# Optimization experiments

Hardware: AMD Instinct MI355X
Metric: run time of the kernel (lower is better)

Reference implementation:

```python
import jax, jax.numpy as jnp
import numpy as np

N = 12288      # nodes
E = 393216     # edges (avg degree 32)
D_IN = 512
D_H = 256      # interm_dim
D_Z = 64       # latent_dim


def setup_inputs() -> dict:
    key = jax.random.key(0)
    ks = jax.random.split(key, 9)
    X = jax.random.normal(ks[0], (N, D_IN), jnp.float32)
    edge_index = jax.random.randint(ks[1], (2, E), 0, N, dtype=jnp.int64)
    # GCNConv weights (glorot-ish scaling)
    W1 = jax.random.normal(ks[2], (D_IN, D_H), jnp.float32) / np.sqrt(D_IN)
    b1 = jnp.zeros((D_H,), jnp.float32)
    Wmu = jax.random.normal(ks[3], (D_H, D_Z), jnp.float32) / np.sqrt(D_H)
    bmu = jnp.zeros((D_Z,), jnp.float32)
    Wsig = jax.random.normal(ks[4], (D_H, 1), jnp.float32) / np.sqrt(D_H)
    bsig = jnp.zeros((1,), jnp.float32)
    # reparameterization noise (torch: Normal(0,1).sample(mus.size()))
    eps = jax.random.normal(ks[5], (N, D_Z), jnp.float32)
    return {"X": X, "edge_index": edge_index, "W1": W1, "b1": b1,
            "Wmu": Wmu, "bmu": bmu, "Wsig": Wsig, "bsig": bsig, "eps": eps}


def _gcn_conv(h_in, W, b, src, dst, norm):
    # GCNConv: linear transform then symmetric-normalized aggregation with self-loops
    h = h_in @ W + b                                   # [N, F_out]
    msg = h[src] * norm[src, None]                     # gather + scale
    agg = jax.ops.segment_sum(msg, dst, num_segments=N)
    # self-loop contribution: norm_i * norm_i * h_i
    return norm[:, None] * (agg + norm[:, None] * h)


def reference(X, edge_index, W1, b1, Wmu, bmu, Wsig, bsig, eps):
    src, dst = edge_index[0], edge_index[1]
    # degree of A + I (edge weight 1, plus self loop)
    deg = jax.ops.segment_sum(jnp.ones((E,), X.dtype), dst, num_segments=N) + 1.0
    norm = jax.lax.rsqrt(deg)                          # D^{-1/2}

    # encoder
    H = jax.nn.relu(_gcn_conv(X, W1, b1, src, dst, norm))   # [N, D_H]; dropout p=0.0
    mus = _gcn_conv(H, Wmu, bmu, src, dst, norm)            # [N, D_Z]
    logsigma2s = _gcn_conv(H, Wsig, bsig, src, dst, norm)   # [N, 1]

    # reparameterize
    sigmas = jnp.exp(0.5 * logsigma2s)                      # [N, 1]
    Z = mus + sigmas * eps                                  # [N, D_Z]

    # dense decoder
    ZZt = Z @ Z.T                                           # [N, N]
    return ZZt, mus, logsigma2s
```

## Files before the change

### kernel.cpp

```cpp
#include <hip/hip_runtime.h>

#define N_NODES 12288
#define N_EDGES 393216
#define DIN 512
#define DH 256
#define DZ 64

typedef __bf16 bf16x8 __attribute__((ext_vector_type(8)));
typedef float f32x4 __attribute__((ext_vector_type(4)));
typedef unsigned short u16x8 __attribute__((ext_vector_type(8)));

static __device__ __forceinline__ unsigned short f2bf(float f) {
    unsigned int u = __float_as_uint(f);
    unsigned int r = (u + 0x7fffu + ((u >> 16) & 1u)) >> 16;
    return (unsigned short)r;
}
static __device__ __forceinline__ float bf2f(unsigned short u) {
    return __uint_as_float((unsigned int)u << 16);
}

__global__ __launch_bounds__(256) void k_prep(const float* __restrict__ X, unsigned short* __restrict__ Xb,
                                              const float* __restrict__ W1, unsigned short* __restrict__ W1T,
                                              const float* __restrict__ Wmu, unsigned short* __restrict__ WmuT,
                                              const int* __restrict__ dst, int* __restrict__ deg) {
    int b = blockIdx.x;
    if (b < 6144) {
        int i = b * 256 + threadIdx.x;
        float4 v = ((const float4*)X)[i];
        ushort4 o;
        o.x = f2bf(v.x); o.y = f2bf(v.y); o.z = f2bf(v.z); o.w = f2bf(v.w);
        ((ushort4*)Xb)[i] = o;
    } else if (b < 6656) {
        int i = (b - 6144) * 256 + threadIdx.x;
        int c = i >> 9, k = i & 511;
        W1T[i] = f2bf(W1[k * DH + c]);
    } else if (b < 6720) {
        int i = (b - 6656) * 256 + threadIdx.x;
        int c = i >> 8, k = i & 255;
        WmuT[i] = f2bf(Wmu[k * DZ + c]);
    } else {
        int e = (b - 6720) * 256 + threadIdx.x;
        atomicAdd(&deg[dst[e]], 1);
    }
}

__global__ __launch_bounds__(1024) void k_scan(const int* __restrict__ cnt, int* __restrict__ rp,
                                               float* __restrict__ norm, int* __restrict__ cursor) {
    __shared__ int sp[1024];
    int t = threadIdx.x;
    int base = t * 12;
    int loc[12];
    int s = 0;
#pragma unroll
    for (int j = 0; j < 12; ++j) {
        int c = cnt[base + j];
        norm[base + j] = rsqrtf((float)c + 1.0f);
        cursor[base + j] = 0;
        loc[j] = s; s += c;
    }
    sp[t] = s;
    __syncthreads();
    for (int off = 1; off < 1024; off <<= 1) {
        int v = (t >= off) ? sp[t - off] : 0;
        __syncthreads();
        sp[t] += v;
        __syncthreads();
    }
    int pre = (t == 0) ? 0 : sp[t - 1];
#pragma unroll
    for (int j = 0; j < 12; ++j) rp[base + j] = pre + loc[j];
    if (t == 1023) rp[N_NODES] = sp[1023];
}

__global__ __launch_bounds__(512) void k_sg(const unsigned short* __restrict__ Xb,
                                            const unsigned short* __restrict__ W1T,
                                            const float* __restrict__ b1, const float* __restrict__ norm,
                                            unsigned short* __restrict__ g1,
                                            const int* __restrict__ src, const int* __restrict__ dst,
                                            const int* __restrict__ rp, int* __restrict__ cursor,
                                            int* __restrict__ ssrc) {
    if (blockIdx.x < 96) {
        int j = blockIdx.x;
        int wid = threadIdx.x >> 6;
        int lane = threadIdx.x & 63;
        int ln = lane & 15, kg = lane >> 4;
        int rb = (j >> 1) * 256 + (wid >> 1) * 64;
        int cb = (j & 1) * 128 + (wid & 1) * 64;
        f32x4 acc[4][4] = {};
        const unsigned short* xa = Xb + (size_t)(rb + ln) * DIN + kg * 8;
        const unsigned short* wb = W1T + (size_t)(cb + ln) * DIN + kg * 8;
        for (int ks = 0; ks < 16; ++ks) {
            int k0 = ks * 32;
            bf16x8 a[4], b[4];
#pragma unroll
            for (int m = 0; m < 4; ++m) a[m] = *(const bf16x8*)(xa + (size_t)m * 16 * DIN + k0);
#pragma unroll
            for (int n = 0; n < 4; ++n) b[n] = *(const bf16x8*)(wb + (size_t)n * 16 * DIN + k0);
#pragma unroll
            for (int m = 0; m < 4; ++m)
#pragma unroll
                for (int n = 0; n < 4; ++n)
                    acc[m][n] = __builtin_amdgcn_mfma_f32_16x16x32_bf16(a[m], b[n], acc[m][n], 0, 0, 0);
        }
#pragma unroll
        for (int m = 0; m < 4; ++m)
#pragma unroll
            for (int r = 0; r < 4; ++r) {
                int row = rb + m * 16 + kg * 4 + r;
                float ni = norm[row];
#pragma unroll
                for (int n = 0; n < 4; ++n) {
                    int col = cb + n * 16 + ln;
                    g1[(size_t)row * DH + col] = f2bf(ni * (acc[m][n][r] + b1[col]));
                }
            }
    } else {
        int base = (blockIdx.x - 96) * 512 + threadIdx.x;
#pragma unroll
        for (int e = base; e < N_EDGES; e += 192 * 512) {
            int d = dst[e];
            int pos = atomicAdd(&cursor[d], 1);
            ssrc[rp[d] + pos] = src[e];
        }
    }
}

__global__ __launch_bounds__(256) void k_agg1(const unsigned short* __restrict__ g1,
                                              const int* __restrict__ rp, const int* __restrict__ ssrc,
                                              const float* __restrict__ norm, const float* __restrict__ Wsig,
                                              unsigned short* __restrict__ G2, float* __restrict__ tvec,
                                              float* __restrict__ qv) {
    int w = threadIdx.x >> 6;
    int lane = threadIdx.x & 63;
    int half = lane >> 5, lh = lane & 31;
    int i = blockIdx.x * 4 + w;
    int beg = rp[i], end = rp[i + 1];
    int cnt = end - beg;
    int itn = (cnt + 1) >> 1;
    size_t cho = (size_t)lh * 8;
    float a8[8] = {};
    float ssum = 0.f;
#pragma unroll 2
    for (int it = 0; it < itn; ++it) {
        int e = beg + it * 2 + half;
        if (e < end) {
            int s = ssrc[e];
            u16x8 v = *(const u16x8*)(g1 + ((size_t)s << 8) + cho);
            ssum += norm[s];
#pragma unroll
            for (int j = 0; j < 8; ++j) a8[j] += bf2f(v[j]);
        }
    }
    if (half == 0) {
        u16x8 v = *(const u16x8*)(g1 + ((size_t)i << 8) + cho);
#pragma unroll
        for (int j = 0; j < 8; ++j) a8[j] += bf2f(v[j]);
    }
#pragma unroll
    for (int j = 0; j < 8; ++j) a8[j] += __shfl_xor(a8[j], 32);
    ssum += __shfl_xor(ssum, 32);
    float ni = norm[i];
    const float4 ws0 = *(const float4*)(Wsig + cho);
    const float4 ws1 = *(const float4*)(Wsig + cho + 4);
    float g[8];
#pragma unroll
    for (int j = 0; j < 8; ++j) g[j] = ni * fmaxf(ni * a8[j], 0.f);
    float qp = g[0] * ws0.x + g[1] * ws0.y + g[2] * ws0.z + g[3] * ws0.w
             + g[4] * ws1.x + g[5] * ws1.y + g[6] * ws1.z + g[7] * ws1.w;
    if (half == 0) {
        u16x8 o;
#pragma unroll
        for (int j = 0; j < 8; ++j) o[j] = f2bf(g[j]);
        *(u16x8*)(G2 + ((size_t)i << 8) + cho) = o;
    }
#pragma unroll
    for (int m = 16; m >= 1; m >>= 1) qp += __shfl_xor(qp, m);
    if (lane == 0) {
        tvec[i] = ssum + ni;
        qv[i] = qp;
    }
}

__global__ __launch_bounds__(256) void k_gemm2(const unsigned short* __restrict__ G2,
                                               const unsigned short* __restrict__ WmuT,
                                               unsigned short* __restrict__ Pb) {
    int wid = threadIdx.x >> 6;
    int lane = threadIdx.x & 63;
    int ln = lane & 15, kg = lane >> 4;
    int rb = blockIdx.x * 128 + wid * 32;
    f32x4 acc[2][4] = {};
    const unsigned short* xa = G2 + (size_t)(rb + ln) * DH + kg * 8;
    const unsigned short* wb = WmuT + (size_t)ln * DH + kg * 8;
    for (int ks = 0; ks < 8; ++ks) {
        int k0 = ks * 32;
        bf16x8 a[2], b[4];
#pragma unroll
        for (int m = 0; m < 2; ++m) a[m] = *(const bf16x8*)(xa + (size_t)m * 16 * DH + k0);
#pragma unroll
        for (int n = 0; n < 4; ++n) b[n] = *(const bf16x8*)(wb + (size_t)n * 16 * DH + k0);
#pragma unroll
        for (int m = 0; m < 2; ++m)
#pragma unroll
            for (int n = 0; n < 4; ++n)
                acc[m][n] = __builtin_amdgcn_mfma_f32_16x16x32_bf16(a[m], b[n], acc[m][n], 0, 0, 0);
    }
#pragma unroll
    for (int m = 0; m < 2; ++m)
#pragma unroll
        for (int n = 0; n < 4; ++n)
#pragma unroll
            for (int r = 0; r < 4; ++r) {
                int row = rb + m * 16 + kg * 4 + r;
                int col = n * 16 + ln;
                Pb[(size_t)row * DZ + col] = f2bf(acc[m][n][r]);
            }
}

__global__ __launch_bounds__(256) void k_agg2(const unsigned short* __restrict__ Pb,
                                              const float* __restrict__ qv,
                                              const int* __restrict__ rp, const int* __restrict__ ssrc,
                                              const float* __restrict__ norm, const float* __restrict__ tvec,
                                              const float* __restrict__ bmu, const float* __restrict__ bsig,
                                              const float* __restrict__ eps,
                                              float* __restrict__ mus_out, float* __restrict__ logs_out,
                                              unsigned short* __restrict__ Zb) {
    int w = threadIdx.x >> 6;
    int lane = threadIdx.x & 63;
    int grp = lane >> 4, li = lane & 15;
    int i = blockIdx.x * 4 + w;
    int beg = rp[i], end = rp[i + 1];
    int cnt = end - beg;
    int itn = (cnt + 3) >> 2;
    int co = li * 4;
    float a4[4] = {};
    float qa = 0.f;
#pragma unroll 2
    for (int it = 0; it < itn; ++it) {
        int e = beg + it * 4 + grp;
        if (e < end) {
            int s = ssrc[e];
            ushort4 v = *(const ushort4*)(Pb + ((size_t)s << 6) + co);
            qa += qv[s];
            a4[0] += bf2f(v.x); a4[1] += bf2f(v.y); a4[2] += bf2f(v.z); a4[3] += bf2f(v.w);
        }
    }
    if (grp == 0) {
        ushort4 v = *(const ushort4*)(Pb + ((size_t)i << 6) + co);
        qa += qv[i];
        a4[0] += bf2f(v.x); a4[1] += bf2f(v.y); a4[2] += bf2f(v.z); a4[3] += bf2f(v.w);
    }
#pragma unroll
    for (int j = 0; j < 4; ++j) {
        a4[j] += __shfl_xor(a4[j], 16);
        a4[j] += __shfl_xor(a4[j], 32);
    }
    qa += __shfl_xor(qa, 16);
    qa += __shfl_xor(qa, 32);
    float ni = norm[i], tv = tvec[i];
    float ls = ni * (qa + bsig[0] * tv);
    float sig = expf(0.5f * ls);
    if (lane == 0) logs_out[i] = ls;
    if (lane < 16) {
        const float4 bm = *(const float4*)(bmu + co);
        float4 mu;
        mu.x = ni * (a4[0] + bm.x * tv);
        mu.y = ni * (a4[1] + bm.y * tv);
        mu.z = ni * (a4[2] + bm.z * tv);
        mu.w = ni * (a4[3] + bm.w * tv);
        size_t oidx = ((size_t)i << 6) + co;
        *(float4*)(mus_out + oidx) = mu;
        const float4 ep = *(const float4*)(eps + oidx);
        ushort4 z;
        z.x = f2bf(mu.x + sig * ep.x);
        z.y = f2bf(mu.y + sig * ep.y);
        z.z = f2bf(mu.z + sig * ep.z);
        z.w = f2bf(mu.w + sig * ep.w);
        *(ushort4*)(Zb + oidx) = z;
    }
}

#define LPAD 260
__global__ __launch_bounds__(256) void k_zzt(const unsigned short* __restrict__ Zb, float* __restrict__ out) {
    __shared__ float lds[32 * LPAD];
    int w = threadIdx.x >> 6;
    int lane = threadIdx.x & 63;
    int ln = lane & 15, kg = lane >> 4;
    int rb = blockIdx.x * 64;
    int cb = blockIdx.y * 256 + w * 64;
    bf16x8 a[4][2], b[4][2];
#pragma unroll
    for (int m = 0; m < 4; ++m)
#pragma unroll
        for (int kc = 0; kc < 2; ++kc)
            a[m][kc] = *(const bf16x8*)(Zb + (size_t)(rb + m * 16 + ln) * DZ + kc * 32 + kg * 8);
#pragma unroll
    for (int n = 0; n < 4; ++n)
#pragma unroll
        for (int kc = 0; kc < 2; ++kc)
            b[n][kc] = *(const bf16x8*)(Zb + (size_t)(cb + n * 16 + ln) * DZ + kc * 32 + kg * 8);
    f32x4 acc[4][4] = {};
#pragma unroll
    for (int m = 0; m < 4; ++m)
#pragma unroll
        for (int n = 0; n < 4; ++n) {
            acc[m][n] = __builtin_amdgcn_mfma_f32_16x16x32_bf16(a[m][0], b[n][0], acc[m][n], 0, 0, 0);
            acc[m][n] = __builtin_amdgcn_mfma_f32_16x16x32_bf16(a[m][1], b[n][1], acc[m][n], 0, 0, 0);
        }
    int c4 = (threadIdx.x & 63) * 4;
    int rw = threadIdx.x >> 6;
    size_t colbase = (size_t)blockIdx.y * 256 + c4;
#pragma unroll
    for (int p = 0; p < 2; ++p) {
        if (p) __syncthreads();
#pragma unroll
        for (int mm = 0; mm < 2; ++mm) {
            int m = p * 2 + mm;
#pragma unroll
            for (int n = 0; n < 4; ++n)
#pragma unroll
                for (int r = 0; r < 4; ++r)
                    lds[(mm * 16 + kg * 4 + r) * LPAD + w * 64 + n * 16 + ln] = acc[m][n][r];
        }
        __syncthreads();
#pragma unroll
        for (int it = 0; it < 8; ++it) {
            int rl = it * 4 + rw;
            f32x4 v = *(const f32x4*)&lds[rl * LPAD + c4];
            __builtin_nontemporal_store(v, (f32x4*)(out + (size_t)(rb + p * 32 + rl) * N_NODES + colbase));
        }
    }
}

extern "C" void kernel_launch(void* const* d_in, const int* in_sizes, int n_in,
                              void* d_out, int out_size, void* d_ws, size_t ws_size,
                              hipStream_t stream) {
    const float* X = (const float*)d_in[0];
    const int* edge = (const int*)d_in[1];
    const float* W1 = (const float*)d_in[2];
    const float* b1 = (const float*)d_in[3];
    const float* Wmu = (const float*)d_in[4];
    const float* bmu = (const float*)d_in[5];
    const float* Wsig = (const float*)d_in[6];
    const float* bsig = (const float*)d_in[7];
    const float* eps = (const float*)d_in[8];

    const int* esrc = edge;
    const int* edst = edge + N_EDGES;

    char* w = (char*)d_ws;
    int* deg = (int*)w;            w += (size_t)N_NODES * 4;
    int* cursor = (int*)w;         w += (size_t)N_NODES * 4;
    float* norm = (float*)w;       w += (size_t)N_NODES * 4;
    float* tvec = (float*)w;       w += (size_t)N_NODES * 4;
    float* qv = (float*)w;         w += (size_t)N_NODES * 4;
    int* rowptr = (int*)w;         w += (size_t)(N_NODES + 64) * 4;
    int* ssrc = (int*)w;           w += (size_t)N_EDGES * 4;
    unsigned short* Xb = (unsigned short*)w;   w += (size_t)N_NODES * DIN * 2;
    unsigned short* W1T = (unsigned short*)w;  w += (size_t)DIN * DH * 2;
    unsigned short* WmuT = (unsigned short*)w; w += (size_t)DH * DZ * 2;
    unsigned short* g1 = (unsigned short*)w;   w += (size_t)N_NODES * DH * 2;
    unsigned short* G2 = (unsigned short*)w;   w += (size_t)N_NODES * DH * 2;
    unsigned short* Pb = (unsigned short*)w;   w += (size_t)N_NODES * DZ * 2;
    unsigned short* Zb = (unsigned short*)w;   w += (size_t)N_NODES * DZ * 2;

    float* out_zzt = (float*)d_out;
    float* out_mus = out_zzt + (size_t)N_NODES * N_NODES;
    float* out_logs = out_mus + (size_t)N_NODES * DZ;

    (void)hipMemsetAsync(deg, 0, (size_t)N_NODES * 4, stream);
    k_prep<<<8256, 256, 0, stream>>>(X, Xb, W1, W1T, Wmu, WmuT, edst, deg);
    k_scan<<<1, 1024, 0, stream>>>(deg, rowptr, norm, cursor);
    k_sg<<<288, 512, 0, stream>>>(Xb, W1T, b1, norm, g1, esrc, edst, rowptr, cursor, ssrc);
    k_agg1<<<N_NODES / 4, 256, 0, stream>>>(g1, rowptr, ssrc, norm, Wsig, G2, tvec, qv);
    k_gemm2<<<N_NODES / 128, 256, 0, stream>>>(G2, WmuT, Pb);
    k_agg2<<<N_NODES / 4, 256, 0, stream>>>(Pb, qv, rowptr, ssrc, norm, tvec, bmu, bsig, eps,
                                            out_mus, out_logs, Zb);
    k_zzt<<<dim3(N_NODES / 64, N_NODES / 256), 256, 0, stream>>>(Zb, out_zzt);
}
```

Baseline: 267.8 us.

## Fuse layer-1 aggregation with the Wmu projection GEMM via shared memory

The aggregated hidden rows of each block (4 nodes) are staged in LDS instead of being written to a global G2 buffer, and each wave then does a 16x16 MFMA tile of the 256->64 projection directly, writing Pb. This drops one kernel launch and the write and re-read of the N x 256 bf16 intermediate. In exchange, each block does an MFMA on a 16-row tile where only 4 rows are valid, so most of the MFMA work is wasted. WmuT is also re-read from cache by every block, and a block-wide barrier is added after aggregation.

```diff
diff --git a/kernel.cpp b/kernel.cpp
--- a/kernel.cpp
+++ b/kernel.cpp
@@ -125,18 +125,20 @@
     }
 }
 
-__global__ __launch_bounds__(256) void k_agg1(const unsigned short* __restrict__ g1,
-                                              const int* __restrict__ rp, const int* __restrict__ ssrc,
-                                              const float* __restrict__ norm, const float* __restrict__ Wsig,
-                                              unsigned short* __restrict__ G2, float* __restrict__ tvec,
-                                              float* __restrict__ qv) {
+#define LP 264
+__global__ __launch_bounds__(256) void k_ag(const unsigned short* __restrict__ g1,
+                                            const int* __restrict__ rp, const int* __restrict__ ssrc,
+                                            const float* __restrict__ norm, const float* __restrict__ Wsig,
+                                            const unsigned short* __restrict__ WmuT,
+                                            float* __restrict__ tvec, float* __restrict__ qv,
+                                            unsigned short* __restrict__ Pb) {
+    __shared__ unsigned short sM[16][LP];
     int w = threadIdx.x >> 6;
     int lane = threadIdx.x & 63;
     int half = lane >> 5, lh = lane & 31;
     int i = blockIdx.x * 4 + w;
     int beg = rp[i], end = rp[i + 1];
-    int cnt = end - beg;
-    int itn = (cnt + 1) >> 1;
+    int itn = (end - beg + 1) >> 1;
     size_t cho = (size_t)lh * 8;
     float a8[8] = {};
     float ssum = 0.f;
@@ -171,7 +173,7 @@
         u16x8 o;
 #pragma unroll
         for (int j = 0; j < 8; ++j) o[j] = f2bf(g[j]);
-        *(u16x8*)(G2 + ((size_t)i << 8) + cho) = o;
+        *(u16x8*)&sM[w][lh * 8] = o;
     }
 #pragma unroll
     for (int m = 16; m >= 1; m >>= 1) qp += __shfl_xor(qp, m);
@@ -179,41 +181,23 @@
         tvec[i] = ssum + ni;
         qv[i] = qp;
     }
-}
-
-__global__ __launch_bounds__(256) void k_gemm2(const unsigned short* __restrict__ G2,
-                                               const unsigned short* __restrict__ WmuT,
-                                               unsigned short* __restrict__ Pb) {
-    int wid = threadIdx.x >> 6;
-    int lane = threadIdx.x & 63;
-    int ln = lane & 15, kg = lane >> 4;
-    int rb = blockIdx.x * 128 + wid * 32;
-    f32x4 acc[2][4] = {};
-    const unsigned short* xa = G2 + (size_t)(rb + ln) * DH + kg * 8;
-    const unsigned short* wb = WmuT + (size_t)ln * DH + kg * 8;
-    for (int ks = 0; ks < 8; ++ks) {
-        int k0 = ks * 32;
-        bf16x8 a[2], b[4];
-#pragma unroll
-        for (int m = 0; m < 2; ++m) a[m] = *(const bf16x8*)(xa + (size_t)m * 16 * DH + k0);
-#pragma unroll
-        for (int n = 0; n < 4; ++n) b[n] = *(const bf16x8*)(wb + (size_t)n * 16 * DH + k0);
-#pragma unroll
-        for (int m = 0; m < 2; ++m)
-#pragma unroll
-            for (int n = 0; n < 4; ++n)
-                acc[m][n] = __builtin_amdgcn_mfma_f32_16x16x32_bf16(a[m], b[n], acc[m][n], 0, 0, 0);
-    }
-#pragma unroll
-    for (int m = 0; m < 2; ++m)
-#pragma unroll
-        for (int n = 0; n < 4; ++n)
-#pragma unroll
-            for (int r = 0; r < 4; ++r) {
-                int row = rb + m * 16 + kg * 4 + r;
-                int col = n * 16 + ln;
-                Pb[(size_t)row * DZ + col] = f2bf(acc[m][n][r]);
-            }
+    __syncthreads();
+    {
+        int ln = lane & 15, kg = lane >> 4;
+        f32x4 acc = {};
+        const unsigned short* wb = WmuT + (size_t)(w * 16 + ln) * DH + kg * 8;
+#pragma unroll
+        for (int ks = 0; ks < 8; ++ks) {
+            bf16x8 a = *(const bf16x8*)&sM[ln][ks * 32 + kg * 8];
+            bf16x8 b = *(const bf16x8*)(wb + ks * 32);
+            acc = __builtin_amdgcn_mfma_f32_16x16x32_bf16(a, b, acc, 0, 0, 0);
+        }
+        if (kg == 0) {
+#pragma unroll
+            for (int r = 0; r < 4; ++r)
+                Pb[(size_t)(blockIdx.x * 4 + r) * DZ + w * 16 + ln] = f2bf(acc[r]);
+        }
+    }
 }
 
 __global__ __launch_bounds__(256) void k_agg2(const unsigned short* __restrict__ Pb,
@@ -229,8 +213,7 @@
     int grp = lane >> 4, li = lane & 15;
     int i = blockIdx.x * 4 + w;
     int beg = rp[i], end = rp[i + 1];
-    int cnt = end - beg;
-    int itn = (cnt + 3) >> 2;
+    int itn = (end - beg + 3) >> 2;
     int co = li * 4;
     float a4[4] = {};
     float qa = 0.f;
@@ -359,7 +342,6 @@
     unsigned short* W1T = (unsigned short*)w;  w += (size_t)DIN * DH * 2;
     unsigned short* WmuT = (unsigned short*)w; w += (size_t)DH * DZ * 2;
     unsigned short* g1 = (unsigned short*)w;   w += (size_t)N_NODES * DH * 2;
-    unsigned short* G2 = (unsigned short*)w;   w += (size_t)N_NODES * DH * 2;
     unsigned short* Pb = (unsigned short*)w;   w += (size_t)N_NODES * DZ * 2;
     unsigned short* Zb = (unsigned short*)w;   w += (size_t)N_NODES * DZ * 2;
 
@@ -371,8 +353,7 @@
     k_prep<<<8256, 256, 0, stream>>>(X, Xb, W1, W1T, Wmu, WmuT, edst, deg);
     k_scan<<<1, 1024, 0, stream>>>(deg, rowptr, norm, cursor);
     k_sg<<<288, 512, 0, stream>>>(Xb, W1T, b1, norm, g1, esrc, edst, rowptr, cursor, ssrc);
-    k_agg1<<<N_NODES / 4, 256, 0, stream>>>(g1, rowptr, ssrc, norm, Wsig, G2, tvec, qv);
-    k_gemm2<<<N_NODES / 128, 256, 0, stream>>>(G2, WmuT, Pb);
+    k_ag<<<N_NODES / 4, 256, 0, stream>>>(g1, rowptr, ssrc, norm, Wsig, WmuT, tvec, qv, Pb);
     k_agg2<<<N_NODES / 4, 256, 0, stream>>>(Pb, qv, rowptr, ssrc, norm, tvec, bmu, bsig, eps,
                                             out_mus, out_logs, Zb);
     k_zzt<<<dim3(N_NODES / 64, N_NODES / 256), 256, 0, stream>>>(Zb, out_zzt);
```

After: 270.3 us. Within noise of the previous version (+0.9%).

## Fold degree scan into GEMM/scatter kernel with flag-based inter-block sync

Applied to the files above, without the earlier changes.

Removes the separate single-block scan kernel launch. The scan (norm, cursor reset, row pointers) now runs in block 96 of k_sg. The other scatter blocks spin on a global flag before placing edges, while the GEMM blocks compute norm directly from deg. This saves one launch and overlaps the serial scan with the GEMM, but relies on the scan block being scheduled alongside the spinning blocks, which holds for 288 blocks on this GPU.

```diff
diff --git a/kernel.cpp b/kernel.cpp
--- a/kernel.cpp
+++ b/kernel.cpp
@@ -44,41 +44,14 @@
     }
 }
 
-__global__ __launch_bounds__(1024) void k_scan(const int* __restrict__ cnt, int* __restrict__ rp,
-                                               float* __restrict__ norm, int* __restrict__ cursor) {
-    __shared__ int sp[1024];
-    int t = threadIdx.x;
-    int base = t * 12;
-    int loc[12];
-    int s = 0;
-#pragma unroll
-    for (int j = 0; j < 12; ++j) {
-        int c = cnt[base + j];
-        norm[base + j] = rsqrtf((float)c + 1.0f);
-        cursor[base + j] = 0;
-        loc[j] = s; s += c;
-    }
-    sp[t] = s;
-    __syncthreads();
-    for (int off = 1; off < 1024; off <<= 1) {
-        int v = (t >= off) ? sp[t - off] : 0;
-        __syncthreads();
-        sp[t] += v;
-        __syncthreads();
-    }
-    int pre = (t == 0) ? 0 : sp[t - 1];
-#pragma unroll
-    for (int j = 0; j < 12; ++j) rp[base + j] = pre + loc[j];
-    if (t == 1023) rp[N_NODES] = sp[1023];
-}
-
 __global__ __launch_bounds__(512) void k_sg(const unsigned short* __restrict__ Xb,
                                             const unsigned short* __restrict__ W1T,
-                                            const float* __restrict__ b1, const float* __restrict__ norm,
-                                            unsigned short* __restrict__ g1,
+                                            const float* __restrict__ b1, const int* __restrict__ deg,
+                                            float* __restrict__ norm, unsigned short* __restrict__ g1,
                                             const int* __restrict__ src, const int* __restrict__ dst,
-                                            const int* __restrict__ rp, int* __restrict__ cursor,
-                                            int* __restrict__ ssrc) {
+                                            int* __restrict__ rp, int* __restrict__ cursor,
+                                            int* __restrict__ ssrc, int* __restrict__ flag) {
+    __shared__ int sp[512];
     if (blockIdx.x < 96) {
         int j = blockIdx.x;
         int wid = threadIdx.x >> 6;
@@ -107,7 +80,7 @@
 #pragma unroll
             for (int r = 0; r < 4; ++r) {
                 int row = rb + m * 16 + kg * 4 + r;
-                float ni = norm[row];
+                float ni = rsqrtf((float)deg[row] + 1.0f);
 #pragma unroll
                 for (int n = 0; n < 4; ++n) {
                     int col = cb + n * 16 + ln;
@@ -115,7 +88,43 @@
                 }
             }
     } else {
-        int base = (blockIdx.x - 96) * 512 + threadIdx.x;
+        int t = threadIdx.x;
+        if (blockIdx.x == 96) {
+            int base = t * 24;
+            int loc[24];
+            int s = 0;
+#pragma unroll
+            for (int j = 0; j < 24; ++j) {
+                int c = deg[base + j];
+                norm[base + j] = rsqrtf((float)c + 1.0f);
+                cursor[base + j] = 0;
+                loc[j] = s; s += c;
+            }
+            sp[t] = s;
+            __syncthreads();
+            for (int off = 1; off < 512; off <<= 1) {
+                int v = (t >= off) ? sp[t - off] : 0;
+                __syncthreads();
+                sp[t] += v;
+                __syncthreads();
+            }
+            int pre = (t == 0) ? 0 : sp[t - 1];
+#pragma unroll
+            for (int j = 0; j < 24; ++j) rp[base + j] = pre + loc[j];
+            if (t == 511) rp[N_NODES] = sp[511];
+            __threadfence();
+            __syncthreads();
+            if (t == 0)
+                __hip_atomic_store(flag, 1, __ATOMIC_RELEASE, __HIP_MEMORY_SCOPE_AGENT);
+        } else {
+            if (t == 0) {
+                while (__hip_atomic_load(flag, __ATOMIC_RELAXED, __HIP_MEMORY_SCOPE_AGENT) == 0)
+                    __builtin_amdgcn_s_sleep(8);
+                (void)__hip_atomic_load(flag, __ATOMIC_ACQUIRE, __HIP_MEMORY_SCOPE_AGENT);
+            }
+            __syncthreads();
+        }
+        int base = (blockIdx.x - 96) * 512 + t;
 #pragma unroll
         for (int e = base; e < N_EDGES; e += 192 * 512) {
             int d = dst[e];
@@ -135,8 +144,7 @@
     int half = lane >> 5, lh = lane & 31;
     int i = blockIdx.x * 4 + w;
     int beg = rp[i], end = rp[i + 1];
-    int cnt = end - beg;
-    int itn = (cnt + 1) >> 1;
+    int itn = (end - beg + 1) >> 1;
     size_t cho = (size_t)lh * 8;
     float a8[8] = {};
     float ssum = 0.f;
@@ -229,8 +237,7 @@
     int grp = lane >> 4, li = lane & 15;
     int i = blockIdx.x * 4 + w;
     int beg = rp[i], end = rp[i + 1];
-    int cnt = end - beg;
-    int itn = (cnt + 3) >> 2;
+    int itn = (end - beg + 3) >> 2;
     int co = li * 4;
     float a4[4] = {};
     float qa = 0.f;
@@ -348,6 +355,7 @@
     const int* edst = edge + N_EDGES;
 
     char* w = (char*)d_ws;
+    int* flag = (int*)w;           w += 64;
     int* deg = (int*)w;            w += (size_t)N_NODES * 4;
     int* cursor = (int*)w;         w += (size_t)N_NODES * 4;
     float* norm = (float*)w;       w += (size_t)N_NODES * 4;
@@ -367,10 +375,9 @@
     float* out_mus = out_zzt + (size_t)N_NODES * N_NODES;
     float* out_logs = out_mus + (size_t)N_NODES * DZ;
 
-    (void)hipMemsetAsync(deg, 0, (size_t)N_NODES * 4, stream);
+    (void)hipMemsetAsync(d_ws, 0, 64 + (size_t)N_NODES * 4, stream);
     k_prep<<<8256, 256, 0, stream>>>(X, Xb, W1, W1T, Wmu, WmuT, edst, deg);
-    k_scan<<<1, 1024, 0, stream>>>(deg, rowptr, norm, cursor);
-    k_sg<<<288, 512, 0, stream>>>(Xb, W1T, b1, norm, g1, esrc, edst, rowptr, cursor, ssrc);
+    k_sg<<<288, 512, 0, stream>>>(Xb, W1T, b1, deg, norm, g1, esrc, edst, rowptr, cursor, ssrc, flag);
     k_agg1<<<N_NODES / 4, 256, 0, stream>>>(g1, rowptr, ssrc, norm, Wsig, G2, tvec, qv);
     k_gemm2<<<N_NODES / 128, 256, 0, stream>>>(G2, WmuT, Pb);
     k_agg2<<<N_NODES / 4, 256, 0, stream>>>(Pb, qv, rowptr, ssrc, norm, tvec, bmu, bsig, eps,
```

New measurement: 260.3 us. 2.8% less time.
